# Optimization experiments

Measured on AMD Instinct MI355X. Metric: run time of the kernel, lower is better.

Reference implementation:

```python
import jax, jax.numpy as jnp
import numpy as np

HEADS = 8
PATCH = 3
EPS = 1e-6


def conv2d(x, w, b, padding=0, groups=1):
    out = jax.lax.conv_general_dilated(
        x, w, (1, 1), [(padding, padding), (padding, padding)],
        feature_group_count=groups,
        dimension_numbers=("NCHW", "OIHW", "NCHW"))
    return out + b[None, :, None, None]


def unfold(x, p):
    # F.unfold(x, p, padding=(p-1)//2, stride=1) -> [B, C*p*p, H*W]
    B, C, H, W = x.shape
    pad = (p - 1) // 2
    xp = jnp.pad(x, ((0, 0), (0, 0), (pad, pad), (pad, pad)))
    patches = jnp.stack(
        [xp[:, :, i:i + H, j:j + W] for i in range(p) for j in range(p)],
        axis=2)  # [B, C, p*p, H, W] -- channel-major like torch unfold
    return patches.reshape(B, C * p * p, H * W)


def linear_attn(q, k, v):
    # q,k: [B, h, N, Dk]; v: [B, h, N, Dv]; ReLU-feature linear attention
    kv = jnp.einsum("bhnd,bhne->bhde", k, v)          # [B,h,Dk,Dv]
    ksum = jnp.sum(k, axis=2)                          # [B,h,Dk]
    num = jnp.einsum("bhnd,bhde->bhne", q, kv)         # [B,h,N,Dv]
    den = jnp.einsum("bhnd,bhd->bhn", q, ksum)[..., None] + EPS
    return num / den


def attn_block(x, qkv_w, qkv_b, proj_w, proj_b):
    B, C, H, W = x.shape
    qkv = conv2d(x, qkv_w, qkv_b)                      # [B, 3C, H, W]
    q, k, v = jnp.split(qkv, 3, axis=1)
    q = jax.nn.relu(q)
    k = jax.nn.relu(k)
    qp = unfold(q, PATCH)                              # [B, C*p*p, HW]
    kp = unfold(k, PATCH)
    N = H * W
    qh = qp.reshape(B, HEADS, -1, N).transpose(0, 1, 3, 2)  # [B,h,N,Dk]
    kh = kp.reshape(B, HEADS, -1, N).transpose(0, 1, 3, 2)
    vh = v.reshape(B, HEADS, -1, N).transpose(0, 1, 3, 2)   # [B,h,N,Dv]
    o = linear_attn(qh, kh, vh)                        # [B,h,N,Dv]
    o = o.transpose(0, 1, 3, 2).reshape(B, C, H, W)
    return conv2d(o, proj_w, proj_b, padding=1)


def ffn_block(x, w1, b1, dw, db, w2, b2):
    C = x.shape[1]
    h = jax.nn.gelu(conv2d(x, w1, b1), approximate=False)
    h = jax.nn.gelu(conv2d(h, dw, db, padding=1, groups=C), approximate=False)
    return conv2d(h, w2, b2)


def setup_inputs() -> dict:
    key = jax.random.key(0)
    ks = jax.random.split(key, 12)
    C = 64
    B, H, W = 2, 256, 256
    s = 0.05
    return {
        "x": jax.random.normal(ks[0], (B, C, H, W), jnp.float32),
        "qkv_w": jax.random.normal(ks[1], (3 * C, C, 1, 1), jnp.float32) * s,
        "qkv_b": jax.random.normal(ks[2], (3 * C,), jnp.float32) * s,
        "proj_w": jax.random.normal(ks[3], (C, C, 3, 3), jnp.float32) * s,
        "proj_b": jax.random.normal(ks[4], (C,), jnp.float32) * s,
        "ffn1_w": jax.random.normal(ks[5], (C, C, 1, 1), jnp.float32) * s,
        "ffn1_b": jax.random.normal(ks[6], (C,), jnp.float32) * s,
        "dw_w": jax.random.normal(ks[7], (C, 1, 3, 3), jnp.float32) * s,
        "dw_b": jax.random.normal(ks[8], (C,), jnp.float32) * s,
        "ffn2_w": jax.random.normal(ks[9], (C, C, 1, 1), jnp.float32) * s,
        "ffn2_b": jax.random.normal(ks[10], (C,), jnp.float32) * s,
    }


def reference(x, qkv_w, qkv_b, proj_w, proj_b, ffn1_w, ffn1_b, dw_w, dw_b, ffn2_w, ffn2_b):
    x = x + attn_block(x, qkv_w, qkv_b, proj_w, proj_b)
    x = x + ffn_block(x, ffn1_w, ffn1_b, dw_w, dw_b, ffn2_w, ffn2_b)
    return x
```

## Files before the change

kernel.cpp:

```cpp
#include <hip/hip_runtime.h>
#include <hip/hip_bf16.h>

typedef __hip_bfloat16 bf16;
typedef __attribute__((ext_vector_type(8))) short short8;
typedef __attribute__((ext_vector_type(4))) short short4v;
typedef __attribute__((ext_vector_type(4))) float floatx4;

#define NPIX 65536

__device__ __forceinline__ float b2f(bf16 v) { return __bfloat162float(v); }
__device__ __forceinline__ bf16 f2b(float v) { return __float2bfloat16(v); }
__device__ __forceinline__ short f2bs(float v) { bf16 t = __float2bfloat16(v); return *(short*)&t; }
__device__ __forceinline__ float us2f(unsigned short u) {
  union { unsigned int i; float f; } t; t.i = ((unsigned int)u) << 16; return t.f;
}
__device__ __forceinline__ float gelu_f(float v) {
  return 0.5f * v * (1.f + erff(v * 0.7071067811865476f));
}

#define OFF_KV  50331648u
#define OFF_KS  50368512u
#define OFF_WP  50373120u

__global__ void k_pack(const float* __restrict__ pw, bf16* __restrict__ wpack,
                       float* __restrict__ kvz) {
  int i = blockIdx.x * 256 + threadIdx.x;
  if (i < 10368) kvz[i] = 0.f;
  int p = i >> 12, rem = i & 4095;
  int co = rem >> 6, ci = rem & 63;
  wpack[i] = f2b(pw[(co * 64 + ci) * 9 + p]);
}

__device__ __forceinline__ void stage_f32(const float* __restrict__ src, bf16* tile) {
  int tid = threadIdx.x;
  int px = tid & 127, chalf = tid >> 7;
#pragma unroll
  for (int it = 0; it < 8; ++it) {
    int ci0 = it * 8 + chalf * 4;
    short4v w;
#pragma unroll
    for (int j = 0; j < 4; ++j) w[j] = f2bs(src[((size_t)(ci0 + j) << 16) + px]);
    *(short4v*)&tile[px * 72 + ci0] = w;
  }
}

__device__ __forceinline__ void stage_bf16(const bf16* __restrict__ src, bf16* tile) {
  int tid = threadIdx.x;
  int px = tid & 127, chalf = tid >> 7;
  const unsigned short* s = (const unsigned short*)src;
#pragma unroll
  for (int it = 0; it < 8; ++it) {
    int ci0 = it * 8 + chalf * 4;
    short4v w;
#pragma unroll
    for (int j = 0; j < 4; ++j) w[j] = (short)s[((size_t)(ci0 + j) << 16) + px];
    *(short4v*)&tile[px * 72 + ci0] = w;
  }
}

__global__ __launch_bounds__(256) void k_qkv_mfma(const float* __restrict__ x,
                                                  const float* __restrict__ qkv_w,
                                                  const float* __restrict__ qkv_b,
                                                  bf16* __restrict__ qkv) {
  __shared__ __align__(16) bf16 tile[128 * 72];
  int tid = threadIdx.x;
  int wv = tid >> 6, ln = tid & 63;
  int n0 = blockIdx.x << 7, b = blockIdx.y;
  stage_f32(x + ((size_t)b << 22) + n0, tile);

  int m = ln & 15, quad = ln >> 4;
  int co = wv * 16 + m;
  short8 afrag[3][2];
#pragma unroll
  for (int sec = 0; sec < 3; ++sec)
#pragma unroll
    for (int s = 0; s < 2; ++s) {
      short8 af;
#pragma unroll
      for (int j = 0; j < 8; ++j)
        af[j] = f2bs(qkv_w[sec * 4096 + co * 64 + s * 32 + quad * 8 + j]);
      afrag[sec][s] = af;
    }
  __syncthreads();

  floatx4 acc[3][8];
#pragma unroll
  for (int sec = 0; sec < 3; ++sec)
#pragma unroll
    for (int nt = 0; nt < 8; ++nt) acc[sec][nt] = (floatx4){0.f, 0.f, 0.f, 0.f};

#pragma unroll
  for (int s = 0; s < 2; ++s) {
    int base = m * 72 + s * 32 + quad * 8;
#pragma unroll
    for (int nt = 0; nt < 8; ++nt) {
      short8 bfrag = *(const short8*)&tile[base + nt * 16 * 72];
#pragma unroll
      for (int sec = 0; sec < 3; ++sec)
        acc[sec][nt] = __builtin_amdgcn_mfma_f32_16x16x32_bf16(afrag[sec][s], bfrag,
                                                               acc[sec][nt], 0, 0, 0);
    }
  }

  bf16* qb = qkv + ((size_t)(b * 192) << 16);
#pragma unroll
  for (int sec = 0; sec < 3; ++sec) {
    bool relu = (sec < 2);
#pragma unroll
    for (int r = 0; r < 4; ++r) {
      int co_r = wv * 16 + quad * 4 + r;
      float bias = qkv_b[sec * 64 + co_r];
      bf16* op = qb + ((size_t)(sec * 64 + co_r) << 16) + n0;
#pragma unroll
      for (int nt = 0; nt < 8; ++nt) {
        float v = acc[sec][nt][r] + bias;
        if (relu) v = fmaxf(v, 0.f);
        op[nt * 16 + m] = f2b(v);
      }
    }
  }
}

__global__ __launch_bounds__(256) void k_ffn2_mfma(const bf16* __restrict__ qkv,
                                                   const float* __restrict__ w2,
                                                   const float* __restrict__ b2,
                                                   float* __restrict__ out) {
  __shared__ __align__(16) bf16 tile[128 * 72];
  int tid = threadIdx.x;
  int wv = tid >> 6, ln = tid & 63;
  int n0 = blockIdx.x << 7, b = blockIdx.z;
  const bf16* qb = qkv + ((size_t)(b * 192) << 16);
  stage_bf16(qb + ((size_t)64 << 16) + n0, tile);

  int m = ln & 15, quad = ln >> 4;
  int co = wv * 16 + m;
  short8 afrag[2];
#pragma unroll
  for (int s = 0; s < 2; ++s) {
    short8 af;
#pragma unroll
    for (int j = 0; j < 8; ++j) af[j] = f2bs(w2[co * 64 + s * 32 + quad * 8 + j]);
    afrag[s] = af;
  }
  __syncthreads();

  floatx4 acc[8];
#pragma unroll
  for (int nt = 0; nt < 8; ++nt) acc[nt] = (floatx4){0.f, 0.f, 0.f, 0.f};
#pragma unroll
  for (int s = 0; s < 2; ++s) {
    int base = m * 72 + s * 32 + quad * 8;
#pragma unroll
    for (int nt = 0; nt < 8; ++nt) {
      short8 bfrag = *(const short8*)&tile[base + nt * 16 * 72];
      acc[nt] = __builtin_amdgcn_mfma_f32_16x16x32_bf16(afrag[s], bfrag, acc[nt], 0, 0, 0);
    }
  }

#pragma unroll
  for (int r = 0; r < 4; ++r) {
    int co_r = wv * 16 + quad * 4 + r;
    float bias = b2[co_r];
    float* op = out + ((size_t)b << 22) + ((size_t)co_r << 16) + n0;
#pragma unroll
    for (int nt = 0; nt < 8; ++nt) {
      int i = nt * 16 + m;
      op[i] = op[i] + bias + acc[nt][r];
    }
  }
}

template <int CTRL>
__device__ __forceinline__ float dpp_add(float v) {
  int t = __builtin_amdgcn_update_dpp(0, __builtin_bit_cast(int, v), CTRL, 0xf, 0xf, true);
  return v + __builtin_bit_cast(float, t);
}

__device__ __forceinline__ float rowsum16(float v) {
  v = dpp_add<0xB1>(v);
  v = dpp_add<0x4E>(v);
  v = dpp_add<0x141>(v);
  v = dpp_add<0x140>(v);
  return v;
}

__device__ __forceinline__ void loadrow10(const unsigned short* __restrict__ plane,
                                          int y, int x0, float kf[10]) {
  if ((unsigned)y < 256u) {
    const unsigned short* row = plane + y * 256;
    short8 k8 = *(const short8*)&row[x0];
#pragma unroll
    for (int j = 0; j < 8; ++j) kf[1 + j] = us2f((unsigned short)k8[j]);
    kf[0] = (x0 > 0) ? us2f(row[x0 - 1]) : 0.f;
    kf[9] = (x0 + 8 < 256) ? us2f(row[x0 + 8]) : 0.f;
  } else {
#pragma unroll
    for (int j = 0; j < 10; ++j) kf[j] = 0.f;
  }
}

__device__ __forceinline__ void loadrow6(const unsigned short* __restrict__ plane,
                                         int y, int x0, float kf[6]) {
  if ((unsigned)y < 256u) {
    const unsigned short* row = plane + y * 256;
    short4v k4 = *(const short4v*)&row[x0];
#pragma unroll
    for (int j = 0; j < 4; ++j) kf[1 + j] = us2f((unsigned short)k4[j]);
    kf[0] = (x0 > 0) ? us2f(row[x0 - 1]) : 0.f;
    kf[5] = (x0 + 4 < 256) ? us2f(row[x0 + 4]) : 0.f;
  } else {
#pragma unroll
    for (int j = 0; j < 6; ++j) kf[j] = 0.f;
  }
}

__global__ __launch_bounds__(256) void k_stats(const bf16* __restrict__ qkv,
                                               float* __restrict__ kv,
                                               float* __restrict__ ksum) {
  int tid = threadIdx.x;
  int chunk = blockIdx.x, c = blockIdx.y;
  int hz = blockIdx.z, h = hz & 7, b = hz >> 3;
  int r = tid >> 5, xseg = tid & 31;
  int y = (chunk << 3) + r;
  int x0 = xseg << 3;
  const bf16* qb = qkv + ((size_t)(b * 192) << 16);
  const unsigned short* kp = (const unsigned short*)qb + (((size_t)(64 + h * 8 + c)) << 16);
  const unsigned short* vp = (const unsigned short*)qb + (((size_t)(128 + h * 8)) << 16);

  float kf[3][10];
#pragma unroll
  for (int rr = 0; rr < 3; ++rr) loadrow10(kp, y + rr - 1, x0, kf[rr]);

  short8 varr[8];
#pragma unroll
  for (int e = 0; e < 8; ++e)
    varr[e] = *(const short8*)&vp[((size_t)e << 16) + y * 256 + x0];

  __shared__ float red[16][81];
  int r16 = tid >> 4;
  bool wr = (tid & 15) == 0;

#pragma unroll
  for (int rr = 0; rr < 3; ++rr)
#pragma unroll
    for (int t = 0; t < 3; ++t) {
      float s = 0.f;
#pragma unroll
      for (int i = 0; i < 8; ++i) s += kf[rr][i + t];
      s = rowsum16(s);
      if (wr) red[r16][72 + rr * 3 + t] = s;
    }

#pragma unroll
  for (int e = 0; e < 8; ++e) {
    float vf[8];
#pragma unroll
    for (int i = 0; i < 8; ++i) vf[i] = us2f((unsigned short)varr[e][i]);
#pragma unroll
    for (int rr = 0; rr < 3; ++rr)
#pragma unroll
      for (int t = 0; t < 3; ++t) {
        float s = 0.f;
#pragma unroll
        for (int i = 0; i < 8; ++i) s = fmaf(kf[rr][i + t], vf[i], s);
        s = rowsum16(s);
        if (wr) red[r16][(rr * 3 + t) * 8 + e] = s;
      }
  }
  __syncthreads();
  if (tid < 81) {
    float s = 0.f;
#pragma unroll
    for (int j = 0; j < 16; ++j) s += red[j][tid];
    int dbase = (b * 8 + h) * 72 + c * 9;
    if (tid < 72) atomicAdd(&kv[((dbase + (tid >> 3)) << 3) + (tid & 7)], s);
    else atomicAdd(&ksum[dbase + (tid - 72)], s);
  }
}

__global__ __launch_bounds__(256) void k_apply(bf16* __restrict__ qkv,
                                               const float* __restrict__ kv,
                                               const float* __restrict__ ksum) {
  int tid = threadIdx.x;
  int chunk = blockIdx.x, h = blockIdx.y, b = blockIdx.z;
  const float* kvb = kv + (size_t)((b * 8 + h) * 72) * 8;
  const float* ksb = ksum + (b * 8 + h) * 72;
  bf16* qb = qkv + ((size_t)(b * 192) << 16);
  bf16* opx = qb + ((size_t)128 << 16);

  __shared__ float skv[576];
  __shared__ float sks[72];
  for (int i = tid; i < 648; i += 256) {
    if (i < 576) skv[i] = kvb[i];
    else sks[i - 576] = ksb[i - 576];
  }
  __syncthreads();

  int r = tid >> 6, xseg = tid & 63;
  int y = (chunk << 2) + r;
  int x0 = xseg << 2;

  float num[8][4], den[4];
#pragma unroll
  for (int i = 0; i < 4; ++i) {
    den[i] = 0.f;
#pragma unroll
    for (int e = 0; e < 8; ++e) num[e][i] = 0.f;
  }

#pragma unroll 1
  for (int c = 0; c < 8; ++c) {
    const unsigned short* qp = (const unsigned short*)qb + ((size_t)(h * 8 + c) << 16);
    float kf[3][6];
#pragma unroll
    for (int rr = 0; rr < 3; ++rr) loadrow6(qp, y + rr - 1, x0, kf[rr]);
#pragma unroll
    for (int rr = 0; rr < 3; ++rr)
#pragma unroll
      for (int t = 0; t < 3; ++t) {
        int d = c * 9 + rr * 3 + t;
        float ksv = sks[d];
#pragma unroll
        for (int i = 0; i < 4; ++i) den[i] = fmaf(kf[rr][i + t], ksv, den[i]);
#pragma unroll
        for (int e = 0; e < 8; ++e) {
          float kvv = skv[d * 8 + e];
#pragma unroll
          for (int i = 0; i < 4; ++i) num[e][i] = fmaf(kf[rr][i + t], kvv, num[e][i]);
        }
      }
  }

#pragma unroll
  for (int i = 0; i < 4; ++i) {
    float inv = 1.f / (den[i] + 1e-6f);
    int n = y * 256 + x0 + i;
    short8 ov;
#pragma unroll
    for (int e = 0; e < 8; ++e) ov[e] = f2bs(num[e][i] * inv);
    *(short8*)&opx[((size_t)n << 6) + h * 8] = ov;
  }
}

__global__ __launch_bounds__(256) void k_proj_ffn1(bf16* qkv,
                                                   const bf16* __restrict__ wpack,
                                                   const float* __restrict__ proj_b,
                                                   const float* __restrict__ x,
                                                   const float* __restrict__ w1,
                                                   const float* __restrict__ b1,
                                                   float* __restrict__ out) {
  __shared__ __align__(16) bf16 tile[3 * 66 * 64];
  int tid = threadIdx.x;
  int wv = tid >> 6, ln = tid & 63;
  int quarter = blockIdx.x, y = blockIdx.y, b = blockIdx.z;
  const bf16* opx = qkv + ((size_t)(b * 192 + 128) << 16);
  int x0 = quarter << 6;
  int m = ln & 15, quad = ln >> 4;
  int co = wv * 16 + m;
  int co0 = wv * 16 + quad * 4;

  short8 afrag[18];
#pragma unroll
  for (int s = 0; s < 18; ++s) {
    int p = s >> 1;
    int ci0 = (s & 1) * 32 + quad * 8;
    afrag[s] = *(const short8*)&wpack[(p * 64 + co) * 64 + ci0];
  }

  for (int q = tid; q < 1584; q += 256) {
    int slot = q >> 3, sub = q & 7;
    int dyr = slot / 66, px = slot - dyr * 66;
    int gy = y + dyr - 1, gx = x0 + px - 1;
    short8 val = {0, 0, 0, 0, 0, 0, 0, 0};
    if ((unsigned)gy < 256u && (unsigned)gx < 256u)
      val = *(const short8*)&opx[(((size_t)(gy << 8) + gx) << 6) + (sub << 3)];
    int ci0 = (sub ^ (px & 7)) << 3;
    *(short8*)&tile[(slot << 6) + ci0] = val;
  }

  float xv[4][4];
#pragma unroll
  for (int nt = 0; nt < 4; ++nt) {
    int gx = x0 + nt * 16 + m;
#pragma unroll
    for (int r = 0; r < 4; ++r)
      xv[nt][r] = x[((size_t)(b * 64 + co0 + r) << 16) + (y << 8) + gx];
  }
  __syncthreads();

  floatx4 acc[4];
#pragma unroll
  for (int nt = 0; nt < 4; ++nt) acc[nt] = (floatx4){0.f, 0.f, 0.f, 0.f};

#pragma unroll
  for (int s = 0; s < 18; ++s) {
    int p = s >> 1;
    int dyr = p / 3, dx = p % 3;
    int ci0 = (s & 1) * 32 + quad * 8;
    int slot0 = dyr * 66;
#pragma unroll
    for (int nt = 0; nt < 4; ++nt) {
      int px = nt * 16 + m + dx;
      int ci = ci0 ^ ((px & 7) << 3);
      short8 bfrag = *(const short8*)&tile[((slot0 + px) << 6) + ci];
      acc[nt] = __builtin_amdgcn_mfma_f32_16x16x32_bf16(afrag[s], bfrag, acc[nt], 0, 0, 0);
    }
  }

  float bias4[4];
#pragma unroll
  for (int r = 0; r < 4; ++r) bias4[r] = proj_b[co0 + r];

  __syncthreads();

#pragma unroll
  for (int nt = 0; nt < 4; ++nt) {
    int px = nt * 16 + m;
    int gx = x0 + px;
    short4v v4;
#pragma unroll
    for (int r = 0; r < 4; ++r) {
      int co_r = co0 + r;
      size_t idx = ((size_t)(b * 64 + co_r) << 16) + (y << 8) + gx;
      float ov = xv[nt][r] + bias4[r] + acc[nt][r];
      out[idx] = ov;
      v4[r] = f2bs(ov);
    }
    int t2i = px * 64 + (((co0 >> 3) ^ (px & 7)) << 3) + (co0 & 7);
    *(short4v*)&tile[t2i] = v4;
  }
  __syncthreads();

  short8 af1[2];
#pragma unroll
  for (int s = 0; s < 2; ++s) {
    short8 af;
#pragma unroll
    for (int j = 0; j < 8; ++j) af[j] = f2bs(w1[co * 64 + s * 32 + quad * 8 + j]);
    af1[s] = af;
  }
  floatx4 acc1[4];
#pragma unroll
  for (int nt = 0; nt < 4; ++nt) acc1[nt] = (floatx4){0.f, 0.f, 0.f, 0.f};
#pragma unroll
  for (int s = 0; s < 2; ++s) {
    int ci0 = s * 32 + quad * 8;
#pragma unroll
    for (int nt = 0; nt < 4; ++nt) {
      int px = nt * 16 + m;
      int ci = ci0 ^ ((px & 7) << 3);
      short8 bfrag = *(const short8*)&tile[px * 64 + ci];
      acc1[nt] = __builtin_amdgcn_mfma_f32_16x16x32_bf16(af1[s], bfrag, acc1[nt], 0, 0, 0);
    }
  }
  bf16* qb = qkv + ((size_t)(b * 192) << 16);
#pragma unroll
  for (int r = 0; r < 4; ++r) {
    int co_r = co0 + r;
    float bias = b1[co_r];
    bf16* op = qb + ((size_t)co_r << 16) + (y << 8) + x0;
#pragma unroll
    for (int nt = 0; nt < 4; ++nt)
      op[nt * 16 + m] = f2b(gelu_f(acc1[nt][r] + bias));
  }
}

__global__ __launch_bounds__(256) void k_dw(bf16* __restrict__ qkv,
                                            const float* __restrict__ dw_w,
                                            const float* __restrict__ dw_b) {
  int blk = blockIdx.x;
  int b = blockIdx.z;
  int c = blk >> 5;
  int y0 = (blk & 31) << 3;
  int tid = threadIdx.x;
  int r = tid >> 5, xseg = tid & 31;
  int y = y0 + r, x0 = xseg << 3;
  bf16* qb = qkv + ((size_t)(b * 192) << 16);
  const unsigned short* ip = (const unsigned short*)qb + ((size_t)c << 16);

  float w[9];
#pragma unroll
  for (int p = 0; p < 9; ++p) w[p] = dw_w[c * 9 + p];
  float bias = dw_b[c];

  float kf[3][10];
#pragma unroll
  for (int rr = 0; rr < 3; ++rr) loadrow10(ip, y + rr - 1, x0, kf[rr]);

  short8 ov;
#pragma unroll
  for (int i = 0; i < 8; ++i) {
    float acc = bias;
#pragma unroll
    for (int rr = 0; rr < 3; ++rr)
#pragma unroll
      for (int t = 0; t < 3; ++t)
        acc = fmaf(kf[rr][i + t], w[rr * 3 + t], acc);
    ov[i] = f2bs(gelu_f(acc));
  }
  *(short8*)&qb[((size_t)(64 + c) << 16) + y * 256 + x0] = ov;
}

extern "C" void kernel_launch(void* const* d_in, const int* in_sizes, int n_in,
                              void* d_out, int out_size, void* d_ws, size_t ws_size,
                              hipStream_t stream) {
  const float* x      = (const float*)d_in[0];
  const float* qkv_w  = (const float*)d_in[1];
  const float* qkv_b  = (const float*)d_in[2];
  const float* proj_w = (const float*)d_in[3];
  const float* proj_b = (const float*)d_in[4];
  const float* ffn1_w = (const float*)d_in[5];
  const float* ffn1_b = (const float*)d_in[6];
  const float* dw_w   = (const float*)d_in[7];
  const float* dw_b   = (const float*)d_in[8];
  const float* ffn2_w = (const float*)d_in[9];
  const float* ffn2_b = (const float*)d_in[10];
  float* out = (float*)d_out;

  char* ws = (char*)d_ws;
  bf16*  qkvb  = (bf16*)ws;
  float* kvb   = (float*)(ws + OFF_KV);
  float* ksb   = (float*)(ws + OFF_KS);
  bf16*  wpack = (bf16*)(ws + OFF_WP);

  k_pack<<<144, 256, 0, stream>>>(proj_w, wpack, kvb);
  k_qkv_mfma<<<dim3(512, 2), 256, 0, stream>>>(x, qkv_w, qkv_b, qkvb);
  k_stats<<<dim3(32, 8, 16), 256, 0, stream>>>(qkvb, kvb, ksb);
  k_apply<<<dim3(64, 8, 2), 256, 0, stream>>>(qkvb, kvb, ksb);
  k_proj_ffn1<<<dim3(4, 256, 2), 256, 0, stream>>>(qkvb, wpack, proj_b, x,
                                                   ffn1_w, ffn1_b, out);
  k_dw<<<dim3(2048, 1, 2), 256, 0, stream>>>(qkvb, dw_w, dw_b);
  k_ffn2_mfma<<<dim3(512, 1, 2), 256, 0, stream>>>(qkvb, ffn2_w, ffn2_b, out);
}
```

Measured before the change: 246.0 us.

## Fuse depthwise conv + GELU into ffn2 MFMA kernel via LDS tile

Merges the depthwise 3x3 conv with GELU and the second 1x1 FFN conv into one kernel. Each block computes the depthwise output for one row half (128 pixels x 64 channels) straight into an XOR-swizzled LDS tile, then runs the MFMA matmul from that tile. This removes the global write and re-read of the depthwise intermediate and one kernel launch. In exchange, each block redoes 3-row halo loads per channel with uncoalesced-ish per-channel row accesses, and all 64 channels are serialized inside a block.

```diff
diff --git a/kernel.cpp b/kernel.cpp
--- a/kernel.cpp
+++ b/kernel.cpp
@@ -40,20 +40,6 @@
     short4v w;
 #pragma unroll
     for (int j = 0; j < 4; ++j) w[j] = f2bs(src[((size_t)(ci0 + j) << 16) + px]);
-    *(short4v*)&tile[px * 72 + ci0] = w;
-  }
-}
-
-__device__ __forceinline__ void stage_bf16(const bf16* __restrict__ src, bf16* tile) {
-  int tid = threadIdx.x;
-  int px = tid & 127, chalf = tid >> 7;
-  const unsigned short* s = (const unsigned short*)src;
-#pragma unroll
-  for (int it = 0; it < 8; ++it) {
-    int ci0 = it * 8 + chalf * 4;
-    short4v w;
-#pragma unroll
-    for (int j = 0; j < 4; ++j) w[j] = (short)s[((size_t)(ci0 + j) << 16) + px];
     *(short4v*)&tile[px * 72 + ci0] = w;
   }
 }
@@ -117,55 +103,6 @@
         if (relu) v = fmaxf(v, 0.f);
         op[nt * 16 + m] = f2b(v);
       }
-    }
-  }
-}
-
-__global__ __launch_bounds__(256) void k_ffn2_mfma(const bf16* __restrict__ qkv,
-                                                   const float* __restrict__ w2,
-                                                   const float* __restrict__ b2,
-                                                   float* __restrict__ out) {
-  __shared__ __align__(16) bf16 tile[128 * 72];
-  int tid = threadIdx.x;
-  int wv = tid >> 6, ln = tid & 63;
-  int n0 = blockIdx.x << 7, b = blockIdx.z;
-  const bf16* qb = qkv + ((size_t)(b * 192) << 16);
-  stage_bf16(qb + ((size_t)64 << 16) + n0, tile);
-
-  int m = ln & 15, quad = ln >> 4;
-  int co = wv * 16 + m;
-  short8 afrag[2];
-#pragma unroll
-  for (int s = 0; s < 2; ++s) {
-    short8 af;
-#pragma unroll
-    for (int j = 0; j < 8; ++j) af[j] = f2bs(w2[co * 64 + s * 32 + quad * 8 + j]);
-    afrag[s] = af;
-  }
-  __syncthreads();
-
-  floatx4 acc[8];
-#pragma unroll
-  for (int nt = 0; nt < 8; ++nt) acc[nt] = (floatx4){0.f, 0.f, 0.f, 0.f};
-#pragma unroll
-  for (int s = 0; s < 2; ++s) {
-    int base = m * 72 + s * 32 + quad * 8;
-#pragma unroll
-    for (int nt = 0; nt < 8; ++nt) {
-      short8 bfrag = *(const short8*)&tile[base + nt * 16 * 72];
-      acc[nt] = __builtin_amdgcn_mfma_f32_16x16x32_bf16(afrag[s], bfrag, acc[nt], 0, 0, 0);
-    }
-  }
-
-#pragma unroll
-  for (int r = 0; r < 4; ++r) {
-    int co_r = wv * 16 + quad * 4 + r;
-    float bias = b2[co_r];
-    float* op = out + ((size_t)b << 22) + ((size_t)co_r << 16) + n0;
-#pragma unroll
-    for (int nt = 0; nt < 8; ++nt) {
-      int i = nt * 16 + m;
-      op[i] = op[i] + bias + acc[nt][r];
     }
   }
 }
@@ -465,40 +402,88 @@
   }
 }
 
-__global__ __launch_bounds__(256) void k_dw(bf16* __restrict__ qkv,
-                                            const float* __restrict__ dw_w,
-                                            const float* __restrict__ dw_b) {
-  int blk = blockIdx.x;
-  int b = blockIdx.z;
-  int c = blk >> 5;
-  int y0 = (blk & 31) << 3;
+__global__ __launch_bounds__(256) void k_dwffn2(const bf16* __restrict__ qkv,
+                                                const float* __restrict__ dw_w,
+                                                const float* __restrict__ dw_b,
+                                                const float* __restrict__ w2,
+                                                const float* __restrict__ b2,
+                                                float* __restrict__ out) {
+  __shared__ __align__(16) bf16 tile[128 * 64];
   int tid = threadIdx.x;
-  int r = tid >> 5, xseg = tid & 31;
-  int y = y0 + r, x0 = xseg << 3;
-  bf16* qb = qkv + ((size_t)(b * 192) << 16);
-  const unsigned short* ip = (const unsigned short*)qb + ((size_t)c << 16);
-
-  float w[9];
-#pragma unroll
-  for (int p = 0; p < 9; ++p) w[p] = dw_w[c * 9 + p];
-  float bias = dw_b[c];
-
-  float kf[3][10];
-#pragma unroll
-  for (int rr = 0; rr < 3; ++rr) loadrow10(ip, y + rr - 1, x0, kf[rr]);
-
-  short8 ov;
-#pragma unroll
-  for (int i = 0; i < 8; ++i) {
-    float acc = bias;
-#pragma unroll
-    for (int rr = 0; rr < 3; ++rr)
-#pragma unroll
-      for (int t = 0; t < 3; ++t)
-        acc = fmaf(kf[rr][i + t], w[rr * 3 + t], acc);
-    ov[i] = f2bs(gelu_f(acc));
-  }
-  *(short8*)&qb[((size_t)(64 + c) << 16) + y * 256 + x0] = ov;
+  int bx = blockIdx.x, b = blockIdx.z;
+  int y = bx >> 1, half = bx & 1;
+  int x0 = half << 7;
+  const bf16* qb = qkv + ((size_t)(b * 192) << 16);
+
+#pragma unroll 1
+  for (int u = 0; u < 4; ++u) {
+    int id = u * 256 + tid;
+    int ci = id >> 4, xseg = id & 15;
+    int gx0 = x0 + (xseg << 3);
+    const unsigned short* ip = (const unsigned short*)qb + ((size_t)ci << 16);
+
+    float w[9];
+#pragma unroll
+    for (int p = 0; p < 9; ++p) w[p] = dw_w[ci * 9 + p];
+    float bias = dw_b[ci];
+
+    float kf[3][10];
+#pragma unroll
+    for (int rr = 0; rr < 3; ++rr) loadrow10(ip, y + rr - 1, gx0, kf[rr]);
+
+#pragma unroll
+    for (int i = 0; i < 8; ++i) {
+      float acc = bias;
+#pragma unroll
+      for (int rr = 0; rr < 3; ++rr)
+#pragma unroll
+        for (int t = 0; t < 3; ++t)
+          acc = fmaf(kf[rr][i + t], w[rr * 3 + t], acc);
+      int px = (xseg << 3) + i;
+      int addr = (px << 6) + ((((ci >> 3) ^ (px & 7)) << 3) | (ci & 7));
+      tile[addr] = f2b(gelu_f(acc));
+    }
+  }
+  __syncthreads();
+
+  int wv = tid >> 6, ln = tid & 63;
+  int m = ln & 15, quad = ln >> 4;
+  int co = wv * 16 + m;
+  short8 afrag[2];
+#pragma unroll
+  for (int s = 0; s < 2; ++s) {
+    short8 af;
+#pragma unroll
+    for (int j = 0; j < 8; ++j) af[j] = f2bs(w2[co * 64 + s * 32 + quad * 8 + j]);
+    afrag[s] = af;
+  }
+
+  floatx4 acc[8];
+#pragma unroll
+  for (int nt = 0; nt < 8; ++nt) acc[nt] = (floatx4){0.f, 0.f, 0.f, 0.f};
+#pragma unroll
+  for (int s = 0; s < 2; ++s) {
+    int ci0 = s * 32 + quad * 8;
+#pragma unroll
+    for (int nt = 0; nt < 8; ++nt) {
+      int px = nt * 16 + m;
+      int ci = ci0 ^ ((px & 7) << 3);
+      short8 bfrag = *(const short8*)&tile[(px << 6) + ci];
+      acc[nt] = __builtin_amdgcn_mfma_f32_16x16x32_bf16(afrag[s], bfrag, acc[nt], 0, 0, 0);
+    }
+  }
+
+#pragma unroll
+  for (int r = 0; r < 4; ++r) {
+    int co_r = wv * 16 + quad * 4 + r;
+    float bias = b2[co_r];
+    float* op = out + ((size_t)b << 22) + ((size_t)co_r << 16) + (y << 8) + x0;
+#pragma unroll
+    for (int nt = 0; nt < 8; ++nt) {
+      int i = nt * 16 + m;
+      op[i] = op[i] + bias + acc[nt][r];
+    }
+  }
 }
 
 extern "C" void kernel_launch(void* const* d_in, const int* in_sizes, int n_in,
@@ -529,6 +514,6 @@
   k_apply<<<dim3(64, 8, 2), 256, 0, stream>>>(qkvb, kvb, ksb);
   k_proj_ffn1<<<dim3(4, 256, 2), 256, 0, stream>>>(qkvb, wpack, proj_b, x,
                                                    ffn1_w, ffn1_b, out);
-  k_dw<<<dim3(2048, 1, 2), 256, 0, stream>>>(qkvb, dw_w, dw_b);
-  k_ffn2_mfma<<<dim3(512, 1, 2), 256, 0, stream>>>(qkvb, ffn2_w, ffn2_b, out);
-}
+  k_dwffn2<<<dim3(512, 1, 2), 256, 0, stream>>>(qkvb, dw_w, dw_b,
+                                                ffn2_w, ffn2_b, out);
+}
```

Result: no change. 243.8 us (-0.9%).
